# Optimization experiments

Measured on AMD Instinct MI355X. Metric: run time of the kernel, lower is better.

Reference implementation:

```python
import jax, jax.numpy as jnp
import numpy as np

D_MODEL = 512
D_STATE = 16
D_CONV = 4
D_INNER = 1024  # expand_factor * d_model
HEADS = 8
D_K = D_MODEL // HEADS
EPS = 1e-5


def layer_norm(x, g, b):
    mu = jnp.mean(x, axis=-1, keepdims=True)
    var = jnp.var(x, axis=-1, keepdims=True)
    return (x - mu) / jnp.sqrt(var + EPS) * g + b


def silu(x):
    return x * jax.nn.sigmoid(x)


def setup_inputs() -> dict:
    key = jax.random.key(0)
    ks = jax.random.split(key, 20)
    s = 0.02

    def n(k, shape):
        return jax.random.normal(k, shape, jnp.float32) * s

    inp = {
        "x": jax.random.normal(ks[0], (8, 1024, D_MODEL), jnp.float32),
        # Mamba params (Linear weights stored as [in, out])
        "in_proj_w": n(ks[1], (D_MODEL, 2 * D_INNER)),
        "conv_w": n(ks[2], (D_INNER, D_CONV)),
        "conv_b": jnp.zeros((D_INNER,), jnp.float32),
        "x_proj_w": n(ks[3], (D_INNER, 2 * D_STATE)),
        "dt_proj_w": n(ks[4], (D_INNER, D_INNER)),
        "dt_proj_b": jnp.zeros((D_INNER,), jnp.float32),
        "A_log": jnp.log(jnp.arange(1, D_STATE + 1, dtype=jnp.float32)),
        "D": jnp.ones((D_INNER,), jnp.float32),
        "out_proj_w": n(ks[5], (D_INNER, D_MODEL)),
        # attention
        "wq_w": n(ks[6], (D_MODEL, D_MODEL)), "wq_b": jnp.zeros((D_MODEL,), jnp.float32),
        "wk_w": n(ks[7], (D_MODEL, D_MODEL)), "wk_b": jnp.zeros((D_MODEL,), jnp.float32),
        "wv_w": n(ks[8], (D_MODEL, D_MODEL)), "wv_b": jnp.zeros((D_MODEL,), jnp.float32),
        "wo_w": n(ks[9], (D_MODEL, D_MODEL)), "wo_b": jnp.zeros((D_MODEL,), jnp.float32),
        "attn_ln_g": jnp.ones((D_MODEL,), jnp.float32), "attn_ln_b": jnp.zeros((D_MODEL,), jnp.float32),
        # FFN
        "ffn_w1": n(ks[10], (D_MODEL, 4 * D_MODEL)), "ffn_b1": jnp.zeros((4 * D_MODEL,), jnp.float32),
        "ffn_w2": n(ks[11], (4 * D_MODEL, D_MODEL)), "ffn_b2": jnp.zeros((D_MODEL,), jnp.float32),
        # norms
        "norm1_g": jnp.ones((D_MODEL,), jnp.float32), "norm1_b": jnp.zeros((D_MODEL,), jnp.float32),
        "norm2_g": jnp.ones((D_MODEL,), jnp.float32), "norm2_b": jnp.zeros((D_MODEL,), jnp.float32),
        "norm3_g": jnp.ones((D_MODEL,), jnp.float32), "norm3_b": jnp.zeros((D_MODEL,), jnp.float32),
        # gate
        "gate_w": n(ks[12], (2 * D_MODEL, D_MODEL)), "gate_b": jnp.zeros((D_MODEL,), jnp.float32),
    }
    return inp


def selective_scan(u, delta, A, B, C, Dp):
    # u, delta: [b, L, d_inner]; B, C: [b, L, d_state]; A: [d_state]; Dp: [d_inner]
    def step(h, inp):
        u_i, d_i, B_i, C_i = inp
        dA = jnp.exp(d_i[:, None, :] * A[None, :, None])        # [b, S, di]
        h = h * dA + (d_i[:, None, :] * B_i[:, :, None]) * u_i[:, None, :]
        y_i = jnp.sum(h * C_i[:, :, None], axis=1)              # [b, di]
        return h, y_i

    b = u.shape[0]
    h0 = jnp.zeros((b, A.shape[0], u.shape[-1]), u.dtype)
    xs = (u.transpose(1, 0, 2), delta.transpose(1, 0, 2),
          B.transpose(1, 0, 2), C.transpose(1, 0, 2))
    _, ys = jax.lax.scan(step, h0, xs)                          # [L, b, di]
    y = ys.transpose(1, 0, 2)
    return y + u * Dp


def mamba(x, in_proj_w, conv_w, conv_b, x_proj_w, dt_proj_w, dt_proj_b, A_log, Dp, out_proj_w):
    L = x.shape[1]
    xr = x @ in_proj_w
    xm, res = jnp.split(xr, 2, axis=-1)                         # [b, L, di] each
    # causal depthwise conv1d: left pad d_conv-1
    xp = jnp.pad(xm, ((0, 0), (D_CONV - 1, 0), (0, 0)))
    xc = sum(conv_w[:, k] * xp[:, k:k + L, :] for k in range(D_CONV)) + conv_b
    xc = silu(xc)
    BC = xc @ x_proj_w
    B, C = jnp.split(BC, 2, axis=-1)                            # [b, L, d_state]
    delta = jax.nn.softplus(xc @ dt_proj_w + dt_proj_b)
    A = -jnp.exp(A_log)
    y = selective_scan(xc, delta, A, B, C, Dp)
    y = y * silu(res)
    return y @ out_proj_w


def attention(q_in, wq_w, wq_b, wk_w, wk_b, wv_w, wv_b, wo_w, wo_b, ln_g, ln_b):
    b, S, _ = q_in.shape
    Q = (q_in @ wq_w + wq_b).reshape(b, S, HEADS, D_K)
    K = (q_in @ wk_w + wk_b).reshape(b, S, HEADS, D_K)
    V = (q_in @ wv_w + wv_b).reshape(b, S, HEADS, D_K)
    scores = jnp.einsum('bqhd,bkhd->bhqk', Q, K) / np.sqrt(D_K).astype(np.float32)
    w = jax.nn.softmax(scores, axis=-1)
    out = jnp.einsum('bhqk,bkhd->bqhd', w, V).reshape(b, S, D_MODEL)
    out = out @ wo_w + wo_b
    return layer_norm(out + q_in, ln_g, ln_b), w


def reference(x, in_proj_w, conv_w, conv_b, x_proj_w, dt_proj_w, dt_proj_b, A_log, D,
              out_proj_w, wq_w, wq_b, wk_w, wk_b, wv_w, wv_b, wo_w, wo_b,
              attn_ln_g, attn_ln_b, ffn_w1, ffn_b1, ffn_w2, ffn_b2,
              norm1_g, norm1_b, norm2_g, norm2_b, norm3_g, norm3_b, gate_w, gate_b):
    mamba_out = mamba(layer_norm(x, norm1_g, norm1_b), in_proj_w, conv_w, conv_b,
                      x_proj_w, dt_proj_w, dt_proj_b, A_log, D, out_proj_w)
    x = x + mamba_out
    xn = layer_norm(x, norm2_g, norm2_b)
    attn_out, attn_w = attention(xn, wq_w, wq_b, wk_w, wk_b, wv_w, wv_b, wo_w, wo_b,
                                 attn_ln_g, attn_ln_b)
    x = x + attn_out
    combined = jnp.concatenate([mamba_out, attn_out], axis=-1)
    g = jax.nn.sigmoid(combined @ gate_w + gate_b)
    fused = g * mamba_out + (1.0 - g) * attn_out
    x = x + fused
    xn3 = layer_norm(x, norm3_g, norm3_b)
    ffn = jax.nn.gelu(xn3 @ ffn_w1 + ffn_b1) @ ffn_w2 + ffn_b2
    x = x + ffn
    return (x, attn_w)
```

## Files before the change

### kernel.cpp

```cpp
#include <hip/hip_runtime.h>

#define SEQL 1024
#define DMODEL 512
#define DINNER 1024
#define NROWS 8192
#define SEG 64
#define NSEG 16
#define LOG2E 1.4426950408889634f

typedef unsigned short u16;
typedef unsigned int u32;
using bf16x8 = __attribute__((ext_vector_type(8))) short;
using f32x4  = __attribute__((ext_vector_type(4))) float;
using u16x4  = __attribute__((ext_vector_type(4))) unsigned short;
using u16x8  = __attribute__((ext_vector_type(8))) unsigned short;

__device__ __forceinline__ float rcp_fast(float x){ return __builtin_amdgcn_rcpf(x); }
__device__ __forceinline__ float exp_fast(float x){ return __expf(x); }
#if __has_builtin(__builtin_amdgcn_exp2f)
__device__ __forceinline__ float exp2_fast(float x){ return __builtin_amdgcn_exp2f(x); }
#else
__device__ __forceinline__ float exp2_fast(float x){ return __expf(x*0.6931471805599453f); }
#endif
__device__ __forceinline__ float sigmoid_f(float x){ return rcp_fast(1.f+exp_fast(-x)); }
__device__ __forceinline__ float softplus_f(float x){ return fmaxf(x,0.f)+__logf(1.f+exp_fast(-fabsf(x))); }
__device__ __forceinline__ float gelu_f(float x){
  float u2 = 1.5957691216057308f*(x+0.044715f*x*x*x);
  float t = 1.f - 2.f*rcp_fast(1.f+exp_fast(u2));
  return 0.5f*x*(1.f+t);
}
__device__ __forceinline__ u16 f2bf(float f){
  u32 u = __builtin_bit_cast(u32, f);
  return (u16)((u + 0x7FFFu + ((u>>16)&1u)) >> 16);
}
__device__ __forceinline__ float bf2f(u16 h){
  return __builtin_bit_cast(float, (u32)h << 16);
}

typedef __attribute__((address_space(1))) const void g_void;
typedef __attribute__((address_space(3))) void l_void;
__device__ __forceinline__ void gl_lds16(const void* g, void* l){
  __builtin_amdgcn_global_load_lds((g_void*)g, (l_void*)l, 16, 0, 0);
}

struct WtDesc { const float* src; u16* dst; int K; int N; int t0; };
struct WtArgs { WtDesc d[11]; };

__global__ __launch_bounds__(256) void wt_k(WtArgs a)
{
  __shared__ float t[64][65];
  int bid = blockIdx.x;
  int i = 0;
  #pragma unroll
  for (int j=1;j<11;++j) if (bid >= a.d[j].t0) i = j;
  const float* src = a.d[i].src; u16* dst = a.d[i].dst;
  int K = a.d[i].K, N = a.d[i].N;
  int ntN = (N+63)>>6;
  int loc = bid - a.d[i].t0;
  int k0 = (loc / ntN)*64, n0 = (loc % ntN)*64;
  int tr = threadIdx.x>>4, tc = threadIdx.x&15;
  #pragma unroll
  for (int p=0;p<4;++p) {
    int r = p*16 + tr; int c = tc*4;
    if (n0 + c < N) {
      float4 v = *(const float4*)(src + (size_t)(k0+r)*N + n0 + c);
      t[r][c]=v.x; t[r][c+1]=v.y; t[r][c+2]=v.z; t[r][c+3]=v.w;
    }
  }
  __syncthreads();
  #pragma unroll
  for (int p=0;p<4;++p) {
    int n = p*16 + tr; int k = tc*4;
    if (n0 + n < N) {
      u16x4 o = { f2bf(t[k][n]), f2bf(t[k+1][n]), f2bf(t[k+2][n]), f2bf(t[k+3][n]) };
      *(u16x4*)(dst + (size_t)(n0+n)*K + k0 + k) = o;
    }
  }
}

__global__ __launch_bounds__(256) void pack3_k(const float* a, const float* b,
                                               const float* c, float* o)
{
  int t = blockIdx.x*256 + threadIdx.x;
  if (t < 512) o[t] = a[t];
  else if (t < 1024) o[t] = b[t-512];
  else if (t < 1536) o[t] = c[t-1024];
}

template<int AM>
__global__ __launch_bounds__(256) void ln_k(const void* av, const void* bv, float* resid,
                                            const float* g, const float* beta,
                                            float* outf, u16* outb)
{
  const int lane = threadIdx.x & 63;
  const int row = (blockIdx.x<<2) + (threadIdx.x>>6);
  size_t off = (size_t)row*DMODEL + lane*8;
  float v[8];
  if (AM==2) {
    u16x8 va = *(const u16x8*)((const u16*)av + off);
    #pragma unroll
    for (int i=0;i<8;++i) v[i] = bf2f(va[i]);
  } else {
    float4 a0 = *(const float4*)((const float*)av + off);
    float4 a1 = *(const float4*)((const float*)av + off + 4);
    v[0]=a0.x; v[1]=a0.y; v[2]=a0.z; v[3]=a0.w;
    v[4]=a1.x; v[5]=a1.y; v[6]=a1.z; v[7]=a1.w;
  }
  if (AM==1) {
    u16x8 wb = *(const u16x8*)((const u16*)bv + off);
    #pragma unroll
    for (int i=0;i<8;++i) v[i] += bf2f(wb[i]);
  } else if (AM==2) {
    float4 b0 = *(const float4*)((const float*)bv + off);
    float4 b1 = *(const float4*)((const float*)bv + off + 4);
    v[0]+=b0.x; v[1]+=b0.y; v[2]+=b0.z; v[3]+=b0.w;
    v[4]+=b1.x; v[5]+=b1.y; v[6]+=b1.z; v[7]+=b1.w;
  }
  if (resid) {
    float4 r0 = {v[0],v[1],v[2],v[3]};
    float4 r1 = {v[4],v[5],v[6],v[7]};
    *(float4*)(resid + off) = r0;
    *(float4*)(resid + off + 4) = r1;
  }
  float s=0.f, q=0.f;
  #pragma unroll
  for (int i=0;i<8;++i){ s += v[i]; q = fmaf(v[i], v[i], q); }
  #pragma unroll
  for (int o=1;o<64;o<<=1){ s += __shfl_xor(s,o); q += __shfl_xor(q,o); }
  float mean = s*(1.f/512.f);
  float var  = q*(1.f/512.f) - mean*mean;
  float rstd = rsqrtf(var + 1e-5f);
  int c = lane*8;
  float4 g0 = *(const float4*)(g+c);
  float4 g1 = *(const float4*)(g+c+4);
  float4 b0 = *(const float4*)(beta+c);
  float4 b1 = *(const float4*)(beta+c+4);
  float gg[8] = {g0.x,g0.y,g0.z,g0.w,g1.x,g1.y,g1.z,g1.w};
  float bb[8] = {b0.x,b0.y,b0.z,b0.w,b1.x,b1.y,b1.z,b1.w};
  float o8[8];
  #pragma unroll
  for (int i=0;i<8;++i) o8[i] = (v[i]-mean)*rstd*gg[i] + bb[i];
  if (outf) {
    float4 f0 = {o8[0],o8[1],o8[2],o8[3]};
    float4 f1 = {o8[4],o8[5],o8[6],o8[7]};
    *(float4*)(outf + off) = f0;
    *(float4*)(outf + off + 4) = f1;
  }
  if (outb) {
    u16x8 ob = { f2bf(o8[0]),f2bf(o8[1]),f2bf(o8[2]),f2bf(o8[3]),
                 f2bf(o8[4]),f2bf(o8[5]),f2bf(o8[6]),f2bf(o8[7]) };
    *(u16x8*)(outb + off) = ob;
  }
}

template<int EPI, int BMODE, int TM, int TN>
__global__ __launch_bounds__(256) void mm_k(
    const u16* Ab, int lda, const u16* Bb, int ldb,
    void* Cv, int ldc, int M, int N, int K,
    const float* bias, const float* p0, const float* p1, const float* p2,
    const u16* A2b, u16* aux)
{
  constexpr int NI = TM/32;
  constexpr int NJ = TN/32;
  __shared__ u16 As[2][TM][32];
  __shared__ u16 Bs[2][TN][32];
  const int tid = threadIdx.x;
  const int bx = blockIdx.x, by = blockIdx.y;
  float* Cf = (float*)Cv;
  u16* Cb = (u16*)Cv;
  const int row0 = by*TM, col0 = bx*TN;
  const int sr = tid>>2, sc = tid&3;
  const int wv = tid>>6, lane = tid&63;
  const int wr = wv>>1, wc = wv&1;
  const int lr = lane&15, lk = (lane>>4)*8;
  const int lq = lane>>4;

  f32x4 acc[NI][NJ];
  #pragma unroll
  for (int i=0;i<NI;++i)
    #pragma unroll
    for (int j=0;j<NJ;++j)
      acc[i][j] = (f32x4){0.f,0.f,0.f,0.f};

  auto stage = [&](int buf, int k0){
    #pragma unroll
    for (int h=0; h<TM/64; ++h) {
      int row = sr + h*64;
      const u16* src;
      if (BMODE==3) {
        int kk = k0 + sc*8;
        src = (kk < 512) ? Ab + (size_t)(row0+row)*512 + kk
                         : A2b + (size_t)(row0+row)*512 + (kk-512);
      } else {
        src = Ab + (size_t)(row0+row)*lda + k0 + sc*8;
      }
      gl_lds16(src, &As[buf][row][sc*8]);
    }
    #pragma unroll
    for (int h=0; h<TN/64; ++h) {
      int rowb = sr + h*64;
      gl_lds16(Bb + (size_t)(col0+rowb)*ldb + k0 + sc*8, &Bs[buf][rowb][sc*8]);
    }
  };

  const int nt = K/32;
  stage(0, 0);
  __syncthreads();
  for (int t=0; t<nt; ++t) {
    int buf = t&1;
    if (t+1 < nt) stage(buf^1, (t+1)*32);
    bf16x8 fa[NI], fb[NJ];
    #pragma unroll
    for (int i=0;i<NI;++i) fa[i] = *(const bf16x8*)&As[buf][wr*(TM/2) + i*16 + lr][lk];
    #pragma unroll
    for (int j=0;j<NJ;++j) fb[j] = *(const bf16x8*)&Bs[buf][wc*(TN/2) + j*16 + lr][lk];
    #pragma unroll
    for (int i=0;i<NI;++i)
      #pragma unroll
      for (int j=0;j<NJ;++j)
        acc[i][j] = __builtin_amdgcn_mfma_f32_16x16x32_bf16(fa[i], fb[j], acc[i][j], 0,0,0);
    __syncthreads();
  }

  #pragma unroll
  for (int i=0;i<NI;++i) {
    #pragma unroll
    for (int j=0;j<NJ;++j) {
      int col = col0 + wc*(TN/2) + j*16 + lr;
      if (col >= N) continue;
      int rowbase = row0 + wr*(TM/2) + i*16 + lq*4;
      f32x4 v4 = acc[i][j];
      if (EPI==11 && col >= 1024) {
        int c2 = col-1024;
        int b2 = rowbase >> 10;
        int l2 = rowbase & 1023;
        float bv = bias[col];
        u16x4 pk = { f2bf(v4[0]+bv), f2bf(v4[1]+bv), f2bf(v4[2]+bv), f2bf(v4[3]+bv) };
        *(u16x4*)(aux + (size_t)b2*DMODEL*SEQL + (size_t)c2*SEQL + l2) = pk;
        continue;
      }
      #pragma unroll
      for (int r=0;r<4;++r) {
        int row = rowbase + r;
        size_t idx = (size_t)row*ldc + col;
        float v = v4[r];
        if (EPI==3) Cb[idx] = f2bf(gelu_f(v + bias[col]));
        else if (EPI==5) Cf[idx] = v + bias[col] + p0[idx];
        else if (EPI==6) {
          float g = sigmoid_f(v + bias[col]);
          float m  = bf2f(((const u16*)p0)[idx]);
          float at = bf2f(((const u16*)p1)[idx]);
          Cf[idx] = p2[idx] + at + g*m + (1.f-g)*at;
        }
        else if (EPI==7) Cb[idx] = f2bf(v);
        else if (EPI==8) Cb[idx] = f2bf(v + bias[col]);
        else if (EPI==11) {
          size_t i2 = (size_t)(col>>9)*4194304 + (size_t)row*512 + (col&511);
          Cb[i2] = f2bf(v + bias[col]);
        }
        else if (EPI==12) {
          if (col < 32) Cf[(size_t)row*32 + col] = v;
          else aux[(size_t)row*1024 + (col-32)] = f2bf(softplus_f(v + bias[col-32]));
        }
      }
    }
  }
}

__global__ __launch_bounds__(256) void attn_k(const u16* Qb, const u16* Kb,
                                              const u16* VTb, float* AW, u16* Hbb)
{
  __shared__ u16 Qs[32][72];
  __shared__ u16 Ps[32][520];
  __shared__ float smax[4][32];
  __shared__ float ssum[4][32];

  const int tid = threadIdx.x;
  const int w = tid>>6, lane = tid&63;
  const int qt = blockIdx.x, bh = blockIdx.y;
  const int b = bh>>3, h = bh&7;
  const int q0 = qt*32;
  const int lr = lane&15, lg = lane>>4;
  const int rw = lg*4;

  {
    int r = tid>>3, c = (tid&7)*8;
    const u16* src = Qb + ((size_t)(b*1024 + q0 + r))*512 + h*64 + c;
    *(uint4*)&Qs[r][c] = *(const uint4*)src;
  }
  __syncthreads();

  f32x4 acc0[16], acc1[16];
  #pragma unroll
  for (int j=0;j<16;++j){ acc0[j]=(f32x4){0.f,0.f,0.f,0.f}; acc1[j]=(f32x4){0.f,0.f,0.f,0.f}; }
  bf16x8 fa00 = *(const bf16x8*)&Qs[lr][lg*8];
  bf16x8 fa01 = *(const bf16x8*)&Qs[lr][32+lg*8];
  bf16x8 fa10 = *(const bf16x8*)&Qs[16+lr][lg*8];
  bf16x8 fa11 = *(const bf16x8*)&Qs[16+lr][32+lg*8];
  const u16* Kbase = Kb + ((size_t)(b*1024 + w*256))*512 + h*64;
  #pragma unroll
  for (int j=0;j<16;++j){
    const u16* krow = Kbase + (size_t)(j*16 + lr)*512 + lg*8;
    bf16x8 fb0 = *(const bf16x8*)krow;
    bf16x8 fb1 = *(const bf16x8*)(krow+32);
    acc0[j] = __builtin_amdgcn_mfma_f32_16x16x32_bf16(fa00, fb0, acc0[j], 0,0,0);
    acc0[j] = __builtin_amdgcn_mfma_f32_16x16x32_bf16(fa01, fb1, acc0[j], 0,0,0);
    acc1[j] = __builtin_amdgcn_mfma_f32_16x16x32_bf16(fa10, fb0, acc1[j], 0,0,0);
    acc1[j] = __builtin_amdgcn_mfma_f32_16x16x32_bf16(fa11, fb1, acc1[j], 0,0,0);
  }

  float mg0[4] = {-1e30f,-1e30f,-1e30f,-1e30f};
  float mg1[4] = {-1e30f,-1e30f,-1e30f,-1e30f};
  #pragma unroll
  for (int j=0;j<16;++j)
    #pragma unroll
    for (int r=0;r<4;++r){
      mg0[r]=fmaxf(mg0[r],acc0[j][r]);
      mg1[r]=fmaxf(mg1[r],acc1[j][r]);
    }
  #pragma unroll
  for (int o=1;o<16;o<<=1)
    #pragma unroll
    for (int r=0;r<4;++r){
      mg0[r]=fmaxf(mg0[r],__shfl_xor(mg0[r],o));
      mg1[r]=fmaxf(mg1[r],__shfl_xor(mg1[r],o));
    }
  if (lr==0){
    #pragma unroll
    for (int r=0;r<4;++r){ smax[w][rw+r]=mg0[r]; smax[w][16+rw+r]=mg1[r]; }
  }
  __syncthreads();
  #pragma unroll
  for (int r=0;r<4;++r){
    mg0[r] = fmaxf(fmaxf(smax[0][rw+r],smax[1][rw+r]),fmaxf(smax[2][rw+r],smax[3][rw+r]));
    mg1[r] = fmaxf(fmaxf(smax[0][16+rw+r],smax[1][16+rw+r]),fmaxf(smax[2][16+rw+r],smax[3][16+rw+r]));
  }
  const float cs = 0.125f*LOG2E;
  float sg0[4]={0.f,0.f,0.f,0.f}, sg1[4]={0.f,0.f,0.f,0.f};
  #pragma unroll
  for (int j=0;j<16;++j)
    #pragma unroll
    for (int r=0;r<4;++r){
      acc0[j][r]=exp2_fast((acc0[j][r]-mg0[r])*cs); sg0[r]+=acc0[j][r];
      acc1[j][r]=exp2_fast((acc1[j][r]-mg1[r])*cs); sg1[r]+=acc1[j][r];
    }
  #pragma unroll
  for (int o=1;o<16;o<<=1)
    #pragma unroll
    for (int r=0;r<4;++r){
      sg0[r]+=__shfl_xor(sg0[r],o);
      sg1[r]+=__shfl_xor(sg1[r],o);
    }
  if (lr==0){
    #pragma unroll
    for (int r=0;r<4;++r){ ssum[w][rw+r]=sg0[r]; ssum[w][16+rw+r]=sg1[r]; }
  }
  __syncthreads();
  float ig0[4], ig1[4];
  #pragma unroll
  for (int r=0;r<4;++r){
    ig0[r] = rcp_fast(ssum[0][rw+r]+ssum[1][rw+r]+ssum[2][rw+r]+ssum[3][rw+r]);
    ig1[r] = rcp_fast(ssum[0][16+rw+r]+ssum[1][16+rw+r]+ssum[2][16+rw+r]+ssum[3][16+rw+r]);
  }

  f32x4 av0 = (f32x4){0.f,0.f,0.f,0.f};
  f32x4 av1 = (f32x4){0.f,0.f,0.f,0.f};
  const u16* Vbase = VTb + (size_t)b*524288 + (size_t)(h*64 + w*16 + lr)*1024;

  #pragma unroll
  for (int half=0; half<2; ++half){
    if ((w>>1) == half) {
      #pragma unroll
      for (int j=0;j<16;++j){
        int col = (w&1)*256 + j*16 + lr;
        #pragma unroll
        for (int r=0;r<4;++r){
          Ps[rw+r][col]    = f2bf(acc0[j][r]*ig0[r]);
          Ps[16+rw+r][col] = f2bf(acc1[j][r]*ig1[r]);
        }
      }
    }
    __syncthreads();
    #pragma unroll
    for (int ks=0; ks<16; ++ks){
      bf16x8 fb  = *(const bf16x8*)(Vbase + half*512 + ks*32 + lg*8);
      bf16x8 pa0 = *(const bf16x8*)&Ps[lr][ks*32 + lg*8];
      bf16x8 pa1 = *(const bf16x8*)&Ps[16+lr][ks*32 + lg*8];
      av0 = __builtin_amdgcn_mfma_f32_16x16x32_bf16(pa0, fb, av0, 0,0,0);
      av1 = __builtin_amdgcn_mfma_f32_16x16x32_bf16(pa1, fb, av1, 0,0,0);
    }
    {
      float* awbase = AW + (size_t)bh*1048576 + (size_t)q0*1024 + half*512;
      int rowh = tid>>7;
      int c = (tid&127)*4;
      #pragma unroll
      for (int it=0; it<16; ++it) {
        int r = it*2 + rowh;
        u16x4 pv = *(const u16x4*)&Ps[r][c];
        float4 f0 = { bf2f(pv[0]), bf2f(pv[1]), bf2f(pv[2]), bf2f(pv[3]) };
        *(float4*)(awbase + (size_t)r*1024 + c) = f0;
      }
    }
    if (half==0) __syncthreads();
  }

  u16* ob = Hbb + ((size_t)(b*1024 + q0))*512 + h*64 + w*16 + lr;
  #pragma unroll
  for (int r=0;r<4;++r){
    ob[(size_t)(rw+r)*512]    = f2bf(av0[r]);
    ob[(size_t)(16+rw+r)*512] = f2bf(av1[r]);
  }
}

__global__ __launch_bounds__(256) void conv_k(const u16* xrb, const float* cw,
                                              const float* cb, u16* xcb)
{
  int t = blockIdx.x*256 + threadIdx.x;
  int d = (t & 255)*4;
  int row = t >> 8;
  int l = row & (SEQL-1);
  const u16* xmb = xrb + (size_t)(row - l)*2048 + d;
  float wv[4][4];
  #pragma unroll
  for (int dd=0; dd<4; ++dd){
    float4 w = *(const float4*)(cw + (size_t)(d+dd)*4);
    wv[dd][0]=w.x; wv[dd][1]=w.y; wv[dd][2]=w.z; wv[dd][3]=w.w;
  }
  float4 acc = *(const float4*)(cb + d);
  #pragma unroll
  for (int k=0;k<4;++k){
    int ls = l + k - 3;
    if (ls >= 0) {
      u16x4 xv = *(const u16x4*)(xmb + (size_t)ls*2048);
      acc.x += wv[0][k]*bf2f(xv[0]);
      acc.y += wv[1][k]*bf2f(xv[1]);
      acc.z += wv[2][k]*bf2f(xv[2]);
      acc.w += wv[3][k]*bf2f(xv[3]);
    }
  }
  float sx = acc.x*rcp_fast(1.f+exp_fast(-acc.x));
  float sy = acc.y*rcp_fast(1.f+exp_fast(-acc.y));
  float sz = acc.z*rcp_fast(1.f+exp_fast(-acc.z));
  float sw = acc.w*rcp_fast(1.f+exp_fast(-acc.w));
  size_t off = (size_t)row*DINNER + d;
  u16x4 ob = { f2bf(sx), f2bf(sy), f2bf(sz), f2bf(sw) };
  *(u16x4*)(xcb + off) = ob;
}

__global__ __launch_bounds__(256) void scan1_k(const u16* dtb, const u16* ub,
                                               const float* bc, const float* A_log,
                                               float* Pq)
{
  const int tid = threadIdx.x;
  const int d   = blockIdx.x*256 + tid;
  const int seg = blockIdx.y;
  const int b   = blockIdx.z;
  const int l0  = seg*SEG;

  __shared__ float BCs[SEG*32];
  {
    const float4* src = (const float4*)(bc + ((size_t)b*SEQL + l0)*32);
    float4* dst = (float4*)BCs;
    dst[tid]     = src[tid];
    dst[tid+256] = src[tid+256];
  }
  float As2[16];
  #pragma unroll
  for (int s=0;s<16;++s) As2[s] = -expf(A_log[s]) * LOG2E;
  __syncthreads();

  float h[16], P[16];
  #pragma unroll
  for (int s=0;s<16;++s){ h[s]=0.f; P[s]=1.f; }

  size_t base = ((size_t)b*SEQL + l0)*DINNER + d;
  const u16* pdt = dtb + base;
  const u16* pu  = ub  + base;

  u16 dpf[8], upf[8];
  #pragma unroll
  for (int j=0;j<8;++j){ dpf[j]=pdt[(size_t)j*DINNER]; upf[j]=pu[(size_t)j*DINNER]; }
  const u16* pdt_f = pdt + (size_t)8*DINNER;
  const u16* pu_f  = pu  + (size_t)8*DINNER;

  for (int l=0; l<SEG; l+=8) {
    bool pf = (l+8 < SEG);
    #pragma unroll
    for (int j=0;j<8;++j) {
      float dt = bf2f(dpf[j]), u = bf2f(upf[j]);
      if (pf) { dpf[j] = *pdt_f; upf[j] = *pu_f; }
      pdt_f += DINNER; pu_f += DINNER;
      float dtu = dt*u;
      const float* Bs = &BCs[(l+j)*32];
      #pragma unroll
      for (int s=0;s<16;++s) {
        float dA = exp2_fast(dt*As2[s]);
        P[s] *= dA;
        h[s] = fmaf(h[s], dA, dtu*Bs[s]);
      }
    }
  }
  float* out = Pq + (((size_t)b*NSEG + seg)*32)*1024 + d;
  #pragma unroll
  for (int s=0;s<16;++s) {
    out[(size_t)s*1024]      = P[s];
    out[(size_t)(16+s)*1024] = h[s];
  }
}

__global__ __launch_bounds__(256) void scan2_k(const u16* dtb, const u16* ub,
                                               const float* bc, const u16* xrb,
                                               const float* A_log, const float* Dp,
                                               const float* Pq, u16* yb)
{
  const int tid = threadIdx.x;
  const int d   = blockIdx.x*256 + tid;
  const int seg = blockIdx.y;
  const int b   = blockIdx.z;
  const int l0  = seg*SEG;

  __shared__ float BCs[SEG*32];
  {
    const float4* src = (const float4*)(bc + ((size_t)b*SEQL + l0)*32);
    float4* dst = (float4*)BCs;
    dst[tid]     = src[tid];
    dst[tid+256] = src[tid+256];
  }
  float As2[16];
  #pragma unroll
  for (int s=0;s<16;++s) As2[s] = -expf(A_log[s]) * LOG2E;
  float dcoef = Dp[d];
  __syncthreads();

  float h[16];
  #pragma unroll
  for (int s=0;s<16;++s) h[s]=0.f;

  const float* pp = Pq + ((size_t)b*NSEG)*32*1024 + d;
  for (int sg=0; sg<seg; ++sg) {
    const float* q = pp + (size_t)sg*32*1024;
    #pragma unroll
    for (int s=0;s<16;++s)
      h[s] = fmaf(h[s], q[(size_t)s*1024], q[(size_t)(16+s)*1024]);
  }

  size_t rbase = (size_t)b*SEQL + l0;
  const u16* pdt = dtb + rbase*DINNER + d;
  const u16* pu  = ub  + rbase*DINNER + d;
  const u16* pr  = xrb + rbase*2048 + 1024 + d;
  u16*       py  = yb  + rbase*DINNER + d;

  u16 dpf[8], upf[8], rpf[8];
  #pragma unroll
  for (int j=0;j<8;++j){
    dpf[j]=pdt[(size_t)j*DINNER]; upf[j]=pu[(size_t)j*DINNER]; rpf[j]=pr[(size_t)j*2048];
  }
  const u16* pdt_f = pdt + (size_t)8*DINNER;
  const u16* pu_f  = pu  + (size_t)8*DINNER;
  const u16* pr_f  = pr  + (size_t)8*2048;

  for (int l=0; l<SEG; l+=8) {
    bool pf = (l+8 < SEG);
    #pragma unroll
    for (int j=0;j<8;++j) {
      float dt = bf2f(dpf[j]), u = bf2f(upf[j]), rv = bf2f(rpf[j]);
      if (pf) { dpf[j] = *pdt_f; upf[j] = *pu_f; rpf[j] = *pr_f; }
      pdt_f += DINNER; pu_f += DINNER; pr_f += 2048;
      float dtu = dt*u;
      float acc = 0.f;
      const float* Bs = &BCs[(l+j)*32];
      #pragma unroll
      for (int s=0;s<16;++s) {
        float dA = exp2_fast(dt*As2[s]);
        h[s] = fmaf(h[s], dA, dtu*Bs[s]);
        acc  = fmaf(h[s], Bs[16+s], acc);
      }
      float y = fmaf(u, dcoef, acc);
      y *= rv * rcp_fast(1.f + exp2_fast(rv*(-LOG2E)));
      *py = f2bf(y);
      py += DINNER;
    }
  }
}

extern "C" void kernel_launch(void* const* d_in, const int* in_sizes, int n_in,
                              void* d_out, int out_size, void* d_ws, size_t ws_size,
                              hipStream_t stream)
{
  const float* x          = (const float*)d_in[0];
  const float* in_proj_w  = (const float*)d_in[1];
  const float* conv_w     = (const float*)d_in[2];
  const float* conv_b     = (const float*)d_in[3];
  const float* x_proj_w   = (const float*)d_in[4];
  const float* dt_proj_w  = (const float*)d_in[5];
  const float* dt_proj_b  = (const float*)d_in[6];
  const float* A_log      = (const float*)d_in[7];
  const float* Dvec       = (const float*)d_in[8];
  const float* out_proj_w = (const float*)d_in[9];
  const float* wq_w = (const float*)d_in[10]; const float* wq_b = (const float*)d_in[11];
  const float* wk_w = (const float*)d_in[12]; const float* wk_b = (const float*)d_in[13];
  const float* wv_w = (const float*)d_in[14]; const float* wv_b = (const float*)d_in[15];
  const float* wo_w = (const float*)d_in[16]; const float* wo_b = (const float*)d_in[17];
  const float* attn_ln_g = (const float*)d_in[18]; const float* attn_ln_b = (const float*)d_in[19];
  const float* ffn_w1 = (const float*)d_in[20]; const float* ffn_b1 = (const float*)d_in[21];
  const float* ffn_w2 = (const float*)d_in[22]; const float* ffn_b2 = (const float*)d_in[23];
  const float* norm1_g = (const float*)d_in[24]; const float* norm1_b = (const float*)d_in[25];
  const float* norm2_g = (const float*)d_in[26]; const float* norm2_b = (const float*)d_in[27];
  const float* norm3_g = (const float*)d_in[28]; const float* norm3_b = (const float*)d_in[29];
  const float* gate_w  = (const float*)d_in[30]; const float* gate_b  = (const float*)d_in[31];

  float* ws  = (float*)d_ws;
  float* BC   = ws;
  float* X1   = BC  + 262144;
  float* XN2  = X1  + 4194304;
  float* Pq   = XN2 + 4194304;
  u16* WT0 = (u16*)(Pq + 4194304);
  u16* XRb = WT0 + 6324224;
  u16* NB  = XRb + 16777216;
  u16* XCb = NB  + 4194304;
  u16* DTb = XCb + 8388608;
  u16* Yb  = DTb + 8388608;
  float* QKVB = (float*)(Yb + 8388608);

  u16* Qb   = XRb;
  u16* Kb   = XRb + 4194304;
  u16* VTb  = XRb + 8388608;
  u16* Hbb  = XRb + 12582912;
  u16* FHb  = XRb;
  u16* MBb  = XCb;
  u16* ATTb = XCb + 4194304;
  u16* WOUTb= DTb;

  u16* inprojT = WT0;
  u16* xprojT  = inprojT + 1048576;
  u16* dtT     = xprojT  + 32768;
  u16* outT    = dtT     + 1048576;
  u16* wqT     = outT    + 524288;
  u16* wkT     = wqT     + 262144;
  u16* wvT     = wkT     + 262144;
  u16* woT     = wvT     + 262144;
  u16* ffn1T   = woT     + 262144;
  u16* ffn2T   = ffn1T   + 1048576;
  u16* gateT   = ffn2T   + 1048576;

  float* XOUT = (float*)d_out;
  float* AW   = (float*)d_out + 4194304;

  const float* nulf = nullptr;
  u16* nulh = nullptr;

  WtArgs wa;
  wa.d[0]  = { in_proj_w, inprojT, 512, 2048, 0 };
  wa.d[1]  = { x_proj_w,  xprojT, 1024,   32, 256 };
  wa.d[2]  = { dt_proj_w, dtT,    1024, 1024, 272 };
  wa.d[3]  = { out_proj_w,outT,   1024,  512, 528 };
  wa.d[4]  = { wq_w,      wqT,     512,  512, 656 };
  wa.d[5]  = { wk_w,      wkT,     512,  512, 720 };
  wa.d[6]  = { wv_w,      wvT,     512,  512, 784 };
  wa.d[7]  = { wo_w,      woT,     512,  512, 848 };
  wa.d[8]  = { ffn_w1,    ffn1T,   512, 2048, 912 };
  wa.d[9]  = { ffn_w2,    ffn2T,  2048,  512, 1168 };
  wa.d[10] = { gate_w,    gateT,  1024,  512, 1424 };
  wt_k<<<1552, 256, 0, stream>>>(wa);
  pack3_k<<<6, 256, 0, stream>>>(wq_b, wk_b, wv_b, QKVB);

  ln_k<0><<<2048, 256, 0, stream>>>(x, nullptr, nullptr, norm1_g, norm1_b, nullptr, NB);
  mm_k<7,0,128,128><<<dim3(16,64), 256, 0, stream>>>(NB,512, inprojT,512, XRb,2048,
        NROWS,2048,512, nulf,nulf,nulf,nulf,nulh,nulh);
  conv_k<<<NROWS, 256, 0, stream>>>(XRb, conv_w, conv_b, XCb);
  mm_k<12,0,128,128><<<dim3(9,64), 256, 0, stream>>>(XCb,1024, xprojT,1024, BC,32,
        NROWS,1056,1024, dt_proj_b,nulf,nulf,nulf,nulh,DTb);
  scan1_k<<<dim3(4,NSEG-1,8), 256, 0, stream>>>(DTb, XCb, BC, A_log, Pq);
  scan2_k<<<dim3(4,NSEG,8),   256, 0, stream>>>(DTb, XCb, BC, XRb, A_log, Dvec, Pq, Yb);
  mm_k<7,0,64,64><<<dim3(8,128), 256, 0, stream>>>(Yb,1024, outT,1024, MBb,512,
        NROWS,512,1024, nulf,nulf,nulf,nulf,nulh,nulh);
  ln_k<1><<<2048, 256, 0, stream>>>(x, MBb, X1, norm2_g, norm2_b, XN2, NB);
  mm_k<11,0,128,128><<<dim3(12,64), 256, 0, stream>>>(NB,512, wqT,512, Qb,512,
        NROWS,1536,512, QKVB,nulf,nulf,nulf,nulh,VTb);
  attn_k<<<dim3(32,64), 256, 0, stream>>>(Qb, Kb, VTb, AW, Hbb);
  mm_k<8,0,64,64><<<dim3(8,128), 256, 0, stream>>>(Hbb,512, woT,512, WOUTb,512,
        NROWS,512,512, wo_b,nulf,nulf,nulf,nulh,nulh);
  ln_k<2><<<2048, 256, 0, stream>>>(WOUTb, XN2, nullptr, attn_ln_g, attn_ln_b, nullptr, ATTb);
  mm_k<6,3,64,64><<<dim3(8,128), 256, 0, stream>>>(MBb,512, gateT,1024, X1,512,
        NROWS,512,1024, gate_b, (const float*)MBb, (const float*)ATTb, X1, ATTb, nulh);
  ln_k<0><<<2048, 256, 0, stream>>>(X1, nullptr, nullptr, norm3_g, norm3_b, nullptr, NB);
  mm_k<3,0,128,128><<<dim3(16,64), 256, 0, stream>>>(NB,512, ffn1T,512, FHb,2048,
        NROWS,2048,512, ffn_b1,nulf,nulf,nulf,nulh,nulh);
  mm_k<5,0,64,64><<<dim3(8,128), 256, 0, stream>>>(FHb,2048, ffn2T,2048, XOUT,512,
        NROWS,512,2048, ffn_b2, X1,nulf,nulf,nulh,nulh);
}
```

Measured before the change: 579.6 us.

## Halve attention query tile to 16 rows, reorder AW store, add MFMA priority

The attention kernel now processes 16 query rows per block instead of 32, doubling the grid to 64x64 blocks and halving accumulator registers (one f32x4[16] set instead of two). This aims to raise occupancy and balance load, at the cost of re-reading K and V twice as often per query. The attention-weight fp32 store is moved ahead of the PV MFMA loop, and s_setprio brackets the MFMA sections to favour matrix issue over the memory-bound stores from other waves.

```diff
diff --git a/kernel.cpp b/kernel.cpp
--- a/kernel.cpp
+++ b/kernel.cpp
@@ -270,101 +270,83 @@
 __global__ __launch_bounds__(256) void attn_k(const u16* Qb, const u16* Kb,
                                               const u16* VTb, float* AW, u16* Hbb)
 {
-  __shared__ u16 Qs[32][72];
-  __shared__ u16 Ps[32][520];
-  __shared__ float smax[4][32];
-  __shared__ float ssum[4][32];
+  __shared__ u16 Qs[16][72];
+  __shared__ u16 Ps[16][520];
+  __shared__ float smax[4][16];
+  __shared__ float ssum[4][16];
 
   const int tid = threadIdx.x;
   const int w = tid>>6, lane = tid&63;
   const int qt = blockIdx.x, bh = blockIdx.y;
   const int b = bh>>3, h = bh&7;
-  const int q0 = qt*32;
+  const int q0 = qt*16;
   const int lr = lane&15, lg = lane>>4;
   const int rw = lg*4;
 
   {
-    int r = tid>>3, c = (tid&7)*8;
+    int r = tid>>4, c = (tid&15)*4;
     const u16* src = Qb + ((size_t)(b*1024 + q0 + r))*512 + h*64 + c;
-    *(uint4*)&Qs[r][c] = *(const uint4*)src;
+    *(u16x4*)&Qs[r][c] = *(const u16x4*)src;
   }
   __syncthreads();
 
-  f32x4 acc0[16], acc1[16];
-  #pragma unroll
-  for (int j=0;j<16;++j){ acc0[j]=(f32x4){0.f,0.f,0.f,0.f}; acc1[j]=(f32x4){0.f,0.f,0.f,0.f}; }
-  bf16x8 fa00 = *(const bf16x8*)&Qs[lr][lg*8];
-  bf16x8 fa01 = *(const bf16x8*)&Qs[lr][32+lg*8];
-  bf16x8 fa10 = *(const bf16x8*)&Qs[16+lr][lg*8];
-  bf16x8 fa11 = *(const bf16x8*)&Qs[16+lr][32+lg*8];
+  f32x4 acc[16];
+  #pragma unroll
+  for (int j=0;j<16;++j) acc[j] = (f32x4){0.f,0.f,0.f,0.f};
+  bf16x8 fa0 = *(const bf16x8*)&Qs[lr][lg*8];
+  bf16x8 fa1 = *(const bf16x8*)&Qs[lr][32+lg*8];
   const u16* Kbase = Kb + ((size_t)(b*1024 + w*256))*512 + h*64;
+  __builtin_amdgcn_s_setprio(1);
   #pragma unroll
   for (int j=0;j<16;++j){
     const u16* krow = Kbase + (size_t)(j*16 + lr)*512 + lg*8;
     bf16x8 fb0 = *(const bf16x8*)krow;
     bf16x8 fb1 = *(const bf16x8*)(krow+32);
-    acc0[j] = __builtin_amdgcn_mfma_f32_16x16x32_bf16(fa00, fb0, acc0[j], 0,0,0);
-    acc0[j] = __builtin_amdgcn_mfma_f32_16x16x32_bf16(fa01, fb1, acc0[j], 0,0,0);
-    acc1[j] = __builtin_amdgcn_mfma_f32_16x16x32_bf16(fa10, fb0, acc1[j], 0,0,0);
-    acc1[j] = __builtin_amdgcn_mfma_f32_16x16x32_bf16(fa11, fb1, acc1[j], 0,0,0);
-  }
-
-  float mg0[4] = {-1e30f,-1e30f,-1e30f,-1e30f};
-  float mg1[4] = {-1e30f,-1e30f,-1e30f,-1e30f};
+    acc[j] = __builtin_amdgcn_mfma_f32_16x16x32_bf16(fa0, fb0, acc[j], 0,0,0);
+    acc[j] = __builtin_amdgcn_mfma_f32_16x16x32_bf16(fa1, fb1, acc[j], 0,0,0);
+  }
+  __builtin_amdgcn_s_setprio(0);
+
+  float mg[4] = {-1e30f,-1e30f,-1e30f,-1e30f};
   #pragma unroll
   for (int j=0;j<16;++j)
     #pragma unroll
+    for (int r=0;r<4;++r) mg[r]=fmaxf(mg[r],acc[j][r]);
+  #pragma unroll
+  for (int o=1;o<16;o<<=1)
+    #pragma unroll
+    for (int r=0;r<4;++r) mg[r]=fmaxf(mg[r],__shfl_xor(mg[r],o));
+  if (lr==0){
+    #pragma unroll
+    for (int r=0;r<4;++r) smax[w][rw+r]=mg[r];
+  }
+  __syncthreads();
+  #pragma unroll
+  for (int r=0;r<4;++r)
+    mg[r] = fmaxf(fmaxf(smax[0][rw+r],smax[1][rw+r]),fmaxf(smax[2][rw+r],smax[3][rw+r]));
+  const float cs = 0.125f*LOG2E;
+  float sg[4]={0.f,0.f,0.f,0.f};
+  #pragma unroll
+  for (int j=0;j<16;++j)
+    #pragma unroll
     for (int r=0;r<4;++r){
-      mg0[r]=fmaxf(mg0[r],acc0[j][r]);
-      mg1[r]=fmaxf(mg1[r],acc1[j][r]);
+      acc[j][r]=exp2_fast((acc[j][r]-mg[r])*cs); sg[r]+=acc[j][r];
     }
   #pragma unroll
   for (int o=1;o<16;o<<=1)
     #pragma unroll
-    for (int r=0;r<4;++r){
-      mg0[r]=fmaxf(mg0[r],__shfl_xor(mg0[r],o));
-      mg1[r]=fmaxf(mg1[r],__shfl_xor(mg1[r],o));
-    }
+    for (int r=0;r<4;++r) sg[r]+=__shfl_xor(sg[r],o);
   if (lr==0){
     #pragma unroll
-    for (int r=0;r<4;++r){ smax[w][rw+r]=mg0[r]; smax[w][16+rw+r]=mg1[r]; }
+    for (int r=0;r<4;++r) ssum[w][rw+r]=sg[r];
   }
   __syncthreads();
-  #pragma unroll
-  for (int r=0;r<4;++r){
-    mg0[r] = fmaxf(fmaxf(smax[0][rw+r],smax[1][rw+r]),fmaxf(smax[2][rw+r],smax[3][rw+r]));
-    mg1[r] = fmaxf(fmaxf(smax[0][16+rw+r],smax[1][16+rw+r]),fmaxf(smax[2][16+rw+r],smax[3][16+rw+r]));
-  }
-  const float cs = 0.125f*LOG2E;
-  float sg0[4]={0.f,0.f,0.f,0.f}, sg1[4]={0.f,0.f,0.f,0.f};
-  #pragma unroll
-  for (int j=0;j<16;++j)
-    #pragma unroll
-    for (int r=0;r<4;++r){
-      acc0[j][r]=exp2_fast((acc0[j][r]-mg0[r])*cs); sg0[r]+=acc0[j][r];
-      acc1[j][r]=exp2_fast((acc1[j][r]-mg1[r])*cs); sg1[r]+=acc1[j][r];
-    }
-  #pragma unroll
-  for (int o=1;o<16;o<<=1)
-    #pragma unroll
-    for (int r=0;r<4;++r){
-      sg0[r]+=__shfl_xor(sg0[r],o);
-      sg1[r]+=__shfl_xor(sg1[r],o);
-    }
-  if (lr==0){
-    #pragma unroll
-    for (int r=0;r<4;++r){ ssum[w][rw+r]=sg0[r]; ssum[w][16+rw+r]=sg1[r]; }
-  }
-  __syncthreads();
-  float ig0[4], ig1[4];
-  #pragma unroll
-  for (int r=0;r<4;++r){
-    ig0[r] = rcp_fast(ssum[0][rw+r]+ssum[1][rw+r]+ssum[2][rw+r]+ssum[3][rw+r]);
-    ig1[r] = rcp_fast(ssum[0][16+rw+r]+ssum[1][16+rw+r]+ssum[2][16+rw+r]+ssum[3][16+rw+r]);
-  }
-
-  f32x4 av0 = (f32x4){0.f,0.f,0.f,0.f};
-  f32x4 av1 = (f32x4){0.f,0.f,0.f,0.f};
+  float ig[4];
+  #pragma unroll
+  for (int r=0;r<4;++r)
+    ig[r] = rcp_fast(ssum[0][rw+r]+ssum[1][rw+r]+ssum[2][rw+r]+ssum[3][rw+r]);
+
+  f32x4 av = (f32x4){0.f,0.f,0.f,0.f};
   const u16* Vbase = VTb + (size_t)b*524288 + (size_t)(h*64 + w*16 + lr)*1024;
 
   #pragma unroll
@@ -374,42 +356,38 @@
       for (int j=0;j<16;++j){
         int col = (w&1)*256 + j*16 + lr;
         #pragma unroll
-        for (int r=0;r<4;++r){
-          Ps[rw+r][col]    = f2bf(acc0[j][r]*ig0[r]);
-          Ps[16+rw+r][col] = f2bf(acc1[j][r]*ig1[r]);
-        }
+        for (int r=0;r<4;++r)
+          Ps[rw+r][col] = f2bf(acc[j][r]*ig[r]);
       }
     }
     __syncthreads();
-    #pragma unroll
-    for (int ks=0; ks<16; ++ks){
-      bf16x8 fb  = *(const bf16x8*)(Vbase + half*512 + ks*32 + lg*8);
-      bf16x8 pa0 = *(const bf16x8*)&Ps[lr][ks*32 + lg*8];
-      bf16x8 pa1 = *(const bf16x8*)&Ps[16+lr][ks*32 + lg*8];
-      av0 = __builtin_amdgcn_mfma_f32_16x16x32_bf16(pa0, fb, av0, 0,0,0);
-      av1 = __builtin_amdgcn_mfma_f32_16x16x32_bf16(pa1, fb, av1, 0,0,0);
-    }
     {
       float* awbase = AW + (size_t)bh*1048576 + (size_t)q0*1024 + half*512;
       int rowh = tid>>7;
       int c = (tid&127)*4;
       #pragma unroll
-      for (int it=0; it<16; ++it) {
+      for (int it=0; it<8; ++it) {
         int r = it*2 + rowh;
         u16x4 pv = *(const u16x4*)&Ps[r][c];
         float4 f0 = { bf2f(pv[0]), bf2f(pv[1]), bf2f(pv[2]), bf2f(pv[3]) };
         *(float4*)(awbase + (size_t)r*1024 + c) = f0;
       }
     }
+    __builtin_amdgcn_s_setprio(1);
+    #pragma unroll
+    for (int ks=0; ks<16; ++ks){
+      bf16x8 fb  = *(const bf16x8*)(Vbase + half*512 + ks*32 + lg*8);
+      bf16x8 pa  = *(const bf16x8*)&Ps[lr][ks*32 + lg*8];
+      av = __builtin_amdgcn_mfma_f32_16x16x32_bf16(pa, fb, av, 0,0,0);
+    }
+    __builtin_amdgcn_s_setprio(0);
     if (half==0) __syncthreads();
   }
 
   u16* ob = Hbb + ((size_t)(b*1024 + q0))*512 + h*64 + w*16 + lr;
   #pragma unroll
-  for (int r=0;r<4;++r){
-    ob[(size_t)(rw+r)*512]    = f2bf(av0[r]);
-    ob[(size_t)(16+rw+r)*512] = f2bf(av1[r]);
-  }
+  for (int r=0;r<4;++r)
+    ob[(size_t)(rw+r)*512] = f2bf(av[r]);
 }
 
 __global__ __launch_bounds__(256) void conv_k(const u16* xrb, const float* cw,
@@ -677,7 +655,7 @@
   ln_k<1><<<2048, 256, 0, stream>>>(x, MBb, X1, norm2_g, norm2_b, XN2, NB);
   mm_k<11,0,128,128><<<dim3(12,64), 256, 0, stream>>>(NB,512, wqT,512, Qb,512,
         NROWS,1536,512, QKVB,nulf,nulf,nulf,nulh,VTb);
-  attn_k<<<dim3(32,64), 256, 0, stream>>>(Qb, Kb, VTb, AW, Hbb);
+  attn_k<<<dim3(64,64), 256, 0, stream>>>(Qb, Kb, VTb, AW, Hbb);
   mm_k<8,0,64,64><<<dim3(8,128), 256, 0, stream>>>(Hbb,512, woT,512, WOUTb,512,
         NROWS,512,512, wo_b,nulf,nulf,nulf,nulh,nulh);
   ln_k<2><<<2048, 256, 0, stream>>>(WOUTb, XN2, nullptr, attn_ln_g, attn_ln_b, nullptr, ATTb);
```

Result: slower. 633.7 us (+9.3%).
